# Optimization experiments

Measured on AMD Instinct MI355X. Metric: run time of the kernel, lower is better.

Reference implementation:

```python
import jax, jax.numpy as jnp
import numpy as np

VOCAB = 21128; EMBED = 768; D_MODEL = 256; H = 100; NTAGS = 21; B = 32; T = 256


def setup_inputs() -> dict:
    key = jax.random.key(0)
    ks = jax.random.split(key, 18)
    n = lambda k, s, sc=0.05: jax.random.normal(k, s, dtype=jnp.float32) * sc
    return {
        "words": jax.random.randint(ks[0], (B, T), 0, VOCAB),
        "target": jax.random.randint(ks[1], (B, T), 0, NTAGS),
        "embed_table": n(ks[2], (VOCAB, EMBED), 1.0),
        "in_fc_w": n(ks[3], (D_MODEL, EMBED)),
        "in_fc_b": n(ks[4], (D_MODEL,)),
        "Wih0": n(ks[5], (2, 4 * H, D_MODEL)),
        "Whh0": n(ks[6], (2, 4 * H, H)),
        "bih0": n(ks[7], (2, 4 * H)),
        "bhh0": n(ks[8], (2, 4 * H)),
        "Wih1": n(ks[9], (2, 4 * H, 2 * H)),
        "Whh1": n(ks[10], (2, 4 * H, H)),
        "bih1": n(ks[11], (2, 4 * H)),
        "bhh1": n(ks[12], (2, 4 * H)),
        "out_w": n(ks[13], (NTAGS, 2 * H)),
        "out_b": n(ks[14], (NTAGS,)),
        "trans": n(ks[15], (NTAGS, NTAGS)),
        "start_s": n(ks[16], (NTAGS,)),
        "end_s": n(ks[17], (NTAGS,)),
    }


def _lstm_dir(x, Wih, Whh, bih, bhh, reverse):
    # x: (T, B, D); torch LSTM gate order i, f, g, o
    Bsz, Hd = x.shape[1], Whh.shape[1]
    pre = jnp.einsum('tbd,gd->tbg', x, Wih) + bih  # precompute input projection

    def step(carry, p):
        h, c = carry
        g = p + h @ Whh.T + bhh
        i, f, gg, o = jnp.split(g, 4, axis=-1)
        c = jax.nn.sigmoid(f) * c + jax.nn.sigmoid(i) * jnp.tanh(gg)
        h = jax.nn.sigmoid(o) * jnp.tanh(c)
        return (h, c), h

    init = (jnp.zeros((Bsz, Hd), x.dtype), jnp.zeros((Bsz, Hd), x.dtype))
    _, hs = jax.lax.scan(step, init, pre, reverse=reverse)
    return hs


def _bilstm(x, layers):
    h = x
    for (Wih, Whh, bih, bhh) in layers:  # fixed small loop over num_layers
        f = _lstm_dir(h, Wih[0], Whh[0], bih[0], bhh[0], False)
        b = _lstm_dir(h, Wih[1], Whh[1], bih[1], bhh[1], True)
        h = jnp.concatenate([f, b], axis=-1)
    return h


def _crf_loss(logits, tags, mask, trans, start_s, end_s):
    # fastNLP ConditionalRandomField loss: normalizer - gold_score, per batch elem
    lt = jnp.swapaxes(logits, 0, 1)          # (T, B, N)
    tt = tags.T                               # (T, B)
    mt = mask.T.astype(logits.dtype)          # (T, B)
    alpha0 = lt[0] + start_s

    def step(alpha, inp):
        emit, m = inp
        tmp = alpha[:, :, None] + trans[None] + emit[:, None, :]  # (B, N, N)
        new = jax.nn.logsumexp(tmp, axis=1)
        return jnp.where(m[:, None] > 0, new, alpha), None

    alpha, _ = jax.lax.scan(step, alpha0, (lt[1:], mt[1:]))
    normalizer = jax.nn.logsumexp(alpha + end_s, axis=1)  # (B,)

    emit_sc = jnp.take_along_axis(lt, tt[..., None], axis=2)[..., 0] * mt
    trans_sc = trans[tt[:-1], tt[1:]] * mt[1:]
    seq_lens = mask.sum(axis=1)
    last_idx = jnp.maximum(seq_lens - 1, 0)
    last_tags = tags[jnp.arange(tags.shape[0]), last_idx]
    gold = emit_sc.sum(0) + trans_sc.sum(0) + start_s[tt[0]] + end_s[last_tags]
    return normalizer - gold


def reference(words, target, embed_table, in_fc_w, in_fc_b, Wih0, Whh0, bih0, bhh0,
              Wih1, Whh1, bih1, bhh1, out_w, out_b, trans, start_s, end_s):
    mask = words != 0
    x = embed_table[words]                       # (B, T, E)
    x = x @ in_fc_w.T + in_fc_b                  # (B, T, D)
    x = jnp.swapaxes(x, 0, 1)                    # (T, B, D)
    h = _bilstm(x, [(Wih0, Whh0, bih0, bhh0), (Wih1, Whh1, bih1, bhh1)])
    h = jnp.swapaxes(h, 0, 1)                    # (B, T, 2H); dropout is identity at eval
    logits = jax.nn.log_softmax(h @ out_w.T + out_b, axis=-1)
    return _crf_loss(logits, target, mask, trans, start_s, end_s)  # (B,)
```

## Files before the change

kernel.cpp:

```cpp
#include <hip/hip_runtime.h>
#include <hip/hip_bf16.h>

#define VOCAB 21128
#define EMBED 768
#define DMODEL 256
#define HID 100
#define NTAGS 21
#define BB 32
#define TT 256
#define NTOK (BB*TT)

typedef float f32x4 __attribute__((ext_vector_type(4)));
typedef unsigned int u32x4 __attribute__((ext_vector_type(4)));
typedef short s16x8 __attribute__((ext_vector_type(8)));

__device__ __forceinline__ float sigm(float x) { return 1.0f / (1.0f + __expf(-x)); }
__device__ __forceinline__ float tanh_(float x) { return 2.0f / (1.0f + __expf(-2.0f * x)) - 1.0f; }

__device__ __forceinline__ unsigned int bfr(float x) {
    unsigned int u = __float_as_uint(x);
    return (u + 0x7fffu + ((u >> 16) & 1u)) >> 16;
}
__device__ __forceinline__ unsigned int bfpack(float lo, float hi) {
    return (bfr(hi) << 16) | bfr(lo);
}
__device__ __forceinline__ s16x8 asfrag(u32x4 v) {
    union { u32x4 u; s16x8 s; } x; x.u = v; return x.s;
}

#define BAR() do { \
    asm volatile("s_waitcnt lgkmcnt(0)" ::: "memory"); \
    __builtin_amdgcn_s_barrier(); \
    __builtin_amdgcn_sched_barrier(0); \
} while (0)

__global__ __launch_bounds__(256) void gemm_mfma(
    const float* __restrict__ A, int lda,
    const float* __restrict__ B, int ldb,
    const float* __restrict__ bias1, const float* __restrict__ bias2,
    float* __restrict__ C, int ldc,
    int N, int K,
    const int* __restrict__ gatherWords, int permGates)
{
    __shared__ unsigned int As_[2][2048];
    __shared__ unsigned int Bs_[2][1024];

    const int tid = threadIdx.x;
    const int row0 = blockIdx.x * 128;
    const int col0 = blockIdx.y * 64;
    const int lane = tid & 63;
    const int wave = tid >> 6;
    const int wr = wave >> 1, wc = wave & 1;
    const int nsteps = (K + 31) >> 5;

    const float* arow[4]; int aoff[4]; int kqA[4];
    #pragma unroll
    for (int j = 0; j < 4; ++j) {
        int v = tid + 256 * j;
        int row = v >> 3, kq = v & 7;
        int grow = row0 + row;
        const float* ap;
        if (gatherWords) {
            int widx = gatherWords[(grow & 31) * TT + (grow >> 5)];
            ap = A + (size_t)widx * lda;
        } else {
            ap = A + (size_t)grow * lda;
        }
        arow[j] = ap + 4 * kq;
        aoff[j] = (row >> 4) * 256 + (kq >> 1) * 64 + (row & 15) * 4 + (kq & 1) * 2;
        kqA[j] = kq;
    }
    const float* brow[2]; int boff[2]; int bok[2]; int kqB[2];
    #pragma unroll
    for (int j = 0; j < 2; ++j) {
        int v = tid + 256 * j;
        int r = v >> 3, kq = v & 7;
        int gcol = col0 + r;
        bok[j] = (gcol < N);
        int src = bok[j] ? gcol : 0;
        if (permGates && bok[j]) {
            int d2 = (gcol >= 400) ? 1 : 0;
            int rr = gcol - d2 * 400;
            src = d2 * 400 + (rr & 3) * 100 + (rr >> 2);
        }
        brow[j] = B + (size_t)src * ldb + 4 * kq;
        boff[j] = (r >> 4) * 256 + (kq >> 1) * 64 + (r & 15) * 4 + (kq & 1) * 2;
        kqB[j] = kq;
    }

    {
        #pragma unroll
        for (int j = 0; j < 4; ++j) {
            f32x4 v = {0.f,0.f,0.f,0.f};
            if (4 * kqA[j] < K) v = *(const f32x4*)(arow[j]);
            As_[0][aoff[j]]     = bfpack(v.x, v.y);
            As_[0][aoff[j] + 1] = bfpack(v.z, v.w);
        }
        #pragma unroll
        for (int j = 0; j < 2; ++j) {
            f32x4 v = {0.f,0.f,0.f,0.f};
            if (bok[j] && 4 * kqB[j] < K) v = *(const f32x4*)(brow[j]);
            Bs_[0][boff[j]]     = bfpack(v.x, v.y);
            Bs_[0][boff[j] + 1] = bfpack(v.z, v.w);
        }
    }
    BAR();

    f32x4 acc[4][2] = {};

    for (int s = 0; s < nsteps; ++s) {
        const int cur = s & 1, nxt = cur ^ 1;

        f32x4 la[4], lb[2];
        if (s + 1 < nsteps) {
            const int kb = (s + 1) * 32;
            #pragma unroll
            for (int j = 0; j < 4; ++j) {
                la[j] = (f32x4){0.f,0.f,0.f,0.f};
                if (kb + 4 * kqA[j] < K) la[j] = *(const f32x4*)(arow[j] + kb);
            }
            #pragma unroll
            for (int j = 0; j < 2; ++j) {
                lb[j] = (f32x4){0.f,0.f,0.f,0.f};
                if (bok[j] && kb + 4 * kqB[j] < K) lb[j] = *(const f32x4*)(brow[j] + kb);
            }
        }

        u32x4 af[4], bf[2];
        #pragma unroll
        for (int mt = 0; mt < 4; ++mt)
            af[mt] = *(const u32x4*)&As_[cur][(4 * wr + mt) * 256 + lane * 4];
        #pragma unroll
        for (int nt = 0; nt < 2; ++nt)
            bf[nt] = *(const u32x4*)&Bs_[cur][(2 * wc + nt) * 256 + lane * 4];
        #pragma unroll
        for (int mt = 0; mt < 4; ++mt)
            #pragma unroll
            for (int nt = 0; nt < 2; ++nt)
                acc[mt][nt] = __builtin_amdgcn_mfma_f32_16x16x32_bf16(
                    asfrag(af[mt]), asfrag(bf[nt]), acc[mt][nt], 0, 0, 0);

        if (s + 1 < nsteps) {
            #pragma unroll
            for (int j = 0; j < 4; ++j) {
                As_[nxt][aoff[j]]     = bfpack(la[j].x, la[j].y);
                As_[nxt][aoff[j] + 1] = bfpack(la[j].z, la[j].w);
            }
            #pragma unroll
            for (int j = 0; j < 2; ++j) {
                Bs_[nxt][boff[j]]     = bfpack(lb[j].x, lb[j].y);
                Bs_[nxt][boff[j] + 1] = bfpack(lb[j].z, lb[j].w);
            }
        }
        BAR();
    }

    const int r4 = (lane >> 4) * 4;
    const int cl = lane & 15;
    #pragma unroll
    for (int nt = 0; nt < 2; ++nt) {
        int gcol = col0 + (2 * wc + nt) * 16 + cl;
        if (gcol < N) {
            int src = gcol;
            if (permGates) {
                int d2 = (gcol >= 400) ? 1 : 0;
                int rr = gcol - d2 * 400;
                src = d2 * 400 + (rr & 3) * 100 + (rr >> 2);
            }
            float bv = bias1[src];
            if (bias2) bv += bias2[src];
            #pragma unroll
            for (int mt = 0; mt < 4; ++mt) {
                int grow = row0 + (4 * wr + mt) * 16 + r4;
                #pragma unroll
                for (int r = 0; r < 4; ++r)
                    C[(size_t)(grow + r) * ldc + gcol] = acc[mt][nt][r] + bv;
            }
        }
    }
}

#define STASH_FRAG(DD, F, A0,A1,A2,A3) { \
    int tile = 4*wave + DD; if (tile > 24) tile = 24; \
    int row16 = 16*tile + m16; \
    const float* srcp = Whh + (size_t)(dir*400 + (row16 & 3)*100 + (row16 >> 2)) * HID; \
    const int k0 = 32*F + 8*g4; \
    f32x4 fa = {0.f,0.f,0.f,0.f}, fb = {0.f,0.f,0.f,0.f}; \
    if (k0 < HID) fa = *(const f32x4*)(srcp + k0); \
    if (k0 + 4 < HID) fb = *(const f32x4*)(srcp + k0 + 4); \
    unsigned p0 = bfpack(fa.x, fa.y), p1 = bfpack(fa.z, fa.w); \
    unsigned p2 = bfpack(fb.x, fb.y), p3 = bfpack(fb.z, fb.w); \
    asm volatile("v_accvgpr_write_b32 a" #A0 ", %0\n\t" \
                 "v_accvgpr_write_b32 a" #A1 ", %1\n\t" \
                 "v_accvgpr_write_b32 a" #A2 ", %2\n\t" \
                 "v_accvgpr_write_b32 a" #A3 ", %3" \
                 :: "v"(p0), "v"(p1), "v"(p2), "v"(p3) \
                 : "a" #A0, "a" #A1, "a" #A2, "a" #A3); }

#define MF(ACC, BF, A0, A3) \
    asm volatile("v_mfma_f32_16x16x32_bf16 %0, a[" #A0 ":" #A3 "], %1, %0" \
                 : "+v"(ACC) : "v"(BF));

#define LOADCHUNK(K2) { \
    const int s0_ = 16 * (K2); \
    _Pragma("unroll") \
    for (int j = 0; j < 4; ++j) { \
        if (okj[j]) { \
            int tg = dir ? (TT - 1 - (s0_ + sicj[j])) : (s0_ + sicj[j]); \
            rr[j] = *(const f32x4*)(pre + (size_t)(tg * BB + b) * 800 + dir * 400 + 4 * gqj[j]); \
        } \
    } }

#define WRITECHUNK(BUF) { \
    _Pragma("unroll") \
    for (int j = 0; j < 4; ++j) { \
        if (okj[j]) *(f32x4*)&preS[(BUF) * 6400 + sicj[j] * 400 + 4 * gqj[j]] = rr[j]; \
    } }

#define LSTM_STEP(SIC) { \
    const int t_ = dir ? (TT - 1 - (s0 + (SIC))) : (s0 + (SIC)); \
    const u32x4* hb_ = (const u32x4*)&h16[(SIC) & 1][0]; \
    u32x4 bf0 = hb_[g4], bf1 = hb_[4+g4], bf2 = hb_[8+g4], bf3 = hb_[12+g4]; \
    f32x4 p4 = *(const f32x4*)&preS[curbase + (SIC) * 400 + my_po]; \
    f32x4 acc0 = {0.f,0.f,0.f,0.f}, acc1 = {0.f,0.f,0.f,0.f}; \
    f32x4 acc2 = {0.f,0.f,0.f,0.f}, acc3 = {0.f,0.f,0.f,0.f}; \
    asm volatile("s_nop 1"); \
    MF(acc0, bf0, 0, 3)   MF(acc1, bf0, 16, 19) MF(acc2, bf0, 32, 35) MF(acc3, bf0, 48, 51) \
    MF(acc0, bf1, 4, 7)   MF(acc1, bf1, 20, 23) MF(acc2, bf1, 36, 39) MF(acc3, bf1, 52, 55) \
    MF(acc0, bf2, 8, 11)  MF(acc1, bf2, 24, 27) MF(acc2, bf2, 40, 43) MF(acc3, bf2, 56, 59) \
    MF(acc0, bf3, 12, 15) MF(acc1, bf3, 28, 31) MF(acc2, bf3, 44, 47) MF(acc3, bf3, 60, 63) \
    asm volatile("s_nop 7\n\ts_nop 7"); \
    f32x4 sel = (d == 0) ? acc0 : (d == 1) ? acc1 : (d == 2) ? acc2 : acc3; \
    float igt = sigm(sel.x + p4.x); \
    float fgt = sigm(sel.y + p4.y); \
    float ggt = tanh_(sel.z + p4.z); \
    float ogt = sigm(sel.w + p4.w); \
    c = fgt * c + igt * ggt; \
    float h = ogt * tanh_(c); \
    if (writer) { \
        h16[((SIC) + 1) & 1][my_u] = (unsigned short)bfr(h); \
        hout[(size_t)(t_ * BB + b) * 200 + dir * HID + my_u] = h; \
    } \
    BAR(); }

__global__ __launch_bounds__(448, 1) void lstm_mfma(
    const float* __restrict__ pre,
    const float* __restrict__ Whh,
    float* __restrict__ hout)
{
    const int dir = blockIdx.x >> 5;
    const int b = blockIdx.x & 31;
    const int tid = threadIdx.x;
    const int wave = tid >> 6;
    const int lane = tid & 63;
    const int m16 = lane & 15;
    const int g4 = lane >> 4;
    const int d = lane & 3;

    __shared__ alignas(16) unsigned short h16[2][128];
    __shared__ alignas(16) float preS[2 * 6400];

    STASH_FRAG(0,0, 0,1,2,3)    STASH_FRAG(0,1, 4,5,6,7)
    STASH_FRAG(0,2, 8,9,10,11)  STASH_FRAG(0,3, 12,13,14,15)
    STASH_FRAG(1,0, 16,17,18,19) STASH_FRAG(1,1, 20,21,22,23)
    STASH_FRAG(1,2, 24,25,26,27) STASH_FRAG(1,3, 28,29,30,31)
    STASH_FRAG(2,0, 32,33,34,35) STASH_FRAG(2,1, 36,37,38,39)
    STASH_FRAG(2,2, 40,41,42,43) STASH_FRAG(2,3, 44,45,46,47)
    STASH_FRAG(3,0, 48,49,50,51) STASH_FRAG(3,1, 52,53,54,55)
    STASH_FRAG(3,2, 56,57,58,59) STASH_FRAG(3,3, 60,61,62,63)

    if (tid < 128) { h16[0][tid] = 0; h16[1][tid] = 0; }

    int my_tile = 4 * wave + d; if (my_tile > 24) my_tile = 24;
    const int my_u = my_tile * 4 + g4;
    const int my_po = 16 * my_tile + 4 * g4;
    const bool writer = ((lane & 12) == 0) && (wave < 6 || d == 0);

    int sicj[4], gqj[4]; bool okj[4];
    #pragma unroll
    for (int j = 0; j < 4; ++j) {
        int idx = tid + 448 * j;
        okj[j] = (idx < 1600);
        int ic = okj[j] ? idx : 0;
        sicj[j] = ic / 100;
        gqj[j] = ic - 100 * sicj[j];
    }

    float c = 0.f;
    f32x4 rr[4];

    LOADCHUNK(0)
    WRITECHUNK(0)
    LOADCHUNK(1)
    BAR();

    for (int k = 0; k < 16; ++k) {
        const int s0 = 16 * k;
        const int curbase = (k & 1) * 6400;
        LSTM_STEP(0)  LSTM_STEP(1)  LSTM_STEP(2)  LSTM_STEP(3)
        LSTM_STEP(4)  LSTM_STEP(5)  LSTM_STEP(6)  LSTM_STEP(7)
        LSTM_STEP(8)  LSTM_STEP(9)  LSTM_STEP(10) LSTM_STEP(11)
        LSTM_STEP(12) LSTM_STEP(13) LSTM_STEP(14) LSTM_STEP(15)
        if (k < 15) { WRITECHUNK((k & 1) ^ 1) }
        if (k < 14) { LOADCHUNK(k + 2) }
        BAR();
    }
}

__global__ __launch_bounds__(256) void logits_lsm(
    const float* __restrict__ h1,
    const float* __restrict__ out_w,
    const float* __restrict__ out_b,
    float* __restrict__ logits)
{
    const int lane = threadIdx.x & 63;
    const int wid = (blockIdx.x * 256 + threadIdx.x) >> 6;
    const int half = lane >> 5;
    const int n = lane & 31;
    const int i = wid * 2 + half;
    if (i >= NTOK) return;

    float acc = -1e30f;
    if (n < NTAGS) {
        acc = out_b[n];
        const float4* hr = (const float4*)(h1 + (size_t)i * 200);
        const float4* wr = (const float4*)(out_w + (size_t)n * 200);
        #pragma unroll
        for (int e = 0; e < 50; ++e) {
            float4 h4 = hr[e], w4 = wr[e];
            acc += h4.x * w4.x + h4.y * w4.y + h4.z * w4.z + h4.w * w4.w;
        }
    }
    float m = acc;
    for (int off = 16; off > 0; off >>= 1) m = fmaxf(m, __shfl_xor(m, off, 32));
    float ex = (n < NTAGS) ? __expf(acc - m) : 0.f;
    float s = ex;
    for (int off = 16; off > 0; off >>= 1) s += __shfl_xor(s, off, 32);
    if (n < NTAGS) logits[(size_t)i * NTAGS + n] = acc - m - __logf(s);
}

__global__ __launch_bounds__(64) void crf_kernel(
    const float* __restrict__ logits,
    const int* __restrict__ words,
    const int* __restrict__ target,
    const float* __restrict__ trans,
    const float* __restrict__ start_s,
    const float* __restrict__ end_s,
    float* __restrict__ out)
{
    const int b = blockIdx.x;
    const int j = threadIdx.x;

    float tcol[NTAGS];
    #pragma unroll
    for (int i = 0; i < NTAGS; ++i) tcol[i] = (j < NTAGS) ? trans[i * NTAGS + j] : 0.f;

    float alpha = (j < NTAGS) ? (logits[(size_t)(0 * BB + b) * NTAGS + j] + start_s[j]) : -1e30f;

    for (int t = 1; t < TT; ++t) {
        bool mt = (words[b * TT + t] != 0);
        if (mt) {
            float v[NTAGS];
            float mx = -1e30f;
            #pragma unroll
            for (int i2 = 0; i2 < NTAGS; ++i2) {
                float ai = __shfl(alpha, i2, 64);
                v[i2] = ai + tcol[i2];
                mx = fmaxf(mx, v[i2]);
            }
            float s = 0.f;
            #pragma unroll
            for (int i2 = 0; i2 < NTAGS; ++i2) s += __expf(v[i2] - mx);
            float na = mx + __logf(s) + logits[(size_t)(t * BB + b) * NTAGS + j];
            alpha = (j < NTAGS) ? na : -1e30f;
        }
    }

    float val = (j < NTAGS) ? (alpha + end_s[j]) : -1e30f;
    float mx = val;
    for (int off = 32; off > 0; off >>= 1) mx = fmaxf(mx, __shfl_xor(mx, off, 64));
    float s = (j < NTAGS) ? __expf(val - mx) : 0.f;
    for (int off = 32; off > 0; off >>= 1) s += __shfl_xor(s, off, 64);
    float norm = mx + __logf(s);

    float gold = 0.f, slen = 0.f;
    for (int t = j; t < TT; t += 64) {
        int tg = target[b * TT + t];
        bool m = (words[b * TT + t] != 0);
        if (m) {
            gold += logits[(size_t)(t * BB + b) * NTAGS + tg];
            slen += 1.f;
            if (t >= 1) gold += trans[target[b * TT + t - 1] * NTAGS + tg];
        }
    }
    for (int off = 32; off > 0; off >>= 1) {
        gold += __shfl_xor(gold, off, 64);
        slen += __shfl_xor(slen, off, 64);
    }
    if (j == 0) {
        int len = (int)slen;
        int last = (len > 0) ? (len - 1) : 0;
        int last_tag = target[b * TT + last];
        gold += start_s[target[b * TT + 0]] + end_s[last_tag];
        out[b] = norm - gold;
    }
}

extern "C" void kernel_launch(void* const* d_in, const int* in_sizes, int n_in,
                              void* d_out, int out_size, void* d_ws, size_t ws_size,
                              hipStream_t stream) {
    const int*   words   = (const int*)  d_in[0];
    const int*   target  = (const int*)  d_in[1];
    const float* embed   = (const float*)d_in[2];
    const float* in_fc_w = (const float*)d_in[3];
    const float* in_fc_b = (const float*)d_in[4];
    const float* Wih0    = (const float*)d_in[5];
    const float* Whh0    = (const float*)d_in[6];
    const float* bih0    = (const float*)d_in[7];
    const float* bhh0    = (const float*)d_in[8];
    const float* Wih1    = (const float*)d_in[9];
    const float* Whh1    = (const float*)d_in[10];
    const float* bih1    = (const float*)d_in[11];
    const float* bhh1    = (const float*)d_in[12];
    const float* out_w   = (const float*)d_in[13];
    const float* out_b   = (const float*)d_in[14];
    const float* trans   = (const float*)d_in[15];
    const float* start_s = (const float*)d_in[16];
    const float* end_s   = (const float*)d_in[17];
    float* out = (float*)d_out;

    float* ws = (float*)d_ws;
    float* x      = ws;
    float* pre    = ws + 2097152;
    float* h0     = ws + 8650752;
    float* h1     = ws;
    float* logits = ws + 1638400;

    gemm_mfma<<<dim3(64, 4), 256, 0, stream>>>(
        embed, EMBED, in_fc_w, EMBED, in_fc_b, nullptr,
        x, DMODEL, DMODEL, EMBED, words, 0);

    gemm_mfma<<<dim3(64, 13), 256, 0, stream>>>(
        x, DMODEL, Wih0, DMODEL, bih0, bhh0,
        pre, 800, 800, DMODEL, nullptr, 1);

    lstm_mfma<<<64, 448, 0, stream>>>(pre, Whh0, h0);

    gemm_mfma<<<dim3(64, 13), 256, 0, stream>>>(
        h0, 200, Wih1, 200, bih1, bhh1,
        pre, 800, 800, 200, nullptr, 1);

    lstm_mfma<<<64, 448, 0, stream>>>(pre, Whh1, h1);

    logits_lsm<<<NTOK / 8, 256, 0, stream>>>(h1, out_w, out_b, logits);

    crf_kernel<<<BB, 64, 0, stream>>>(logits, words, target, trans, start_s, end_s, out);
}
```

Baseline: 580.6 us.

## Deepen GEMM K-tile, restructure CRF recurrence, template LSTM barrier variant

The GEMM now stages 64-wide K slices instead of 32, halving the number of barrier-separated steps and doubling the MFMAs issued per step, at the cost of double the LDS and more registers. The CRF forward recursion preloads the word mask into registers, prefetches the next timestep's emission, and replaces serial max/sum chains with tree reductions to shorten the dependent latency per step. The LSTM kernel is templated so the second-layer launch drops the sched_barrier after each step's barrier, letting the compiler schedule across it.

```diff
diff --git a/kernel.cpp b/kernel.cpp
--- a/kernel.cpp
+++ b/kernel.cpp
@@ -28,11 +28,12 @@
     union { u32x4 u; s16x8 s; } x; x.u = v; return x.s;
 }
 
-#define BAR() do { \
+#define BARV(SB) do { \
     asm volatile("s_waitcnt lgkmcnt(0)" ::: "memory"); \
     __builtin_amdgcn_s_barrier(); \
-    __builtin_amdgcn_sched_barrier(0); \
+    if (SB) __builtin_amdgcn_sched_barrier(0); \
 } while (0)
+#define BAR() BARV(1)
 
 __global__ __launch_bounds__(256) void gemm_mfma(
     const float* __restrict__ A, int lda,
@@ -42,8 +43,8 @@
     int N, int K,
     const int* __restrict__ gatherWords, int permGates)
 {
-    __shared__ unsigned int As_[2][2048];
-    __shared__ unsigned int Bs_[2][1024];
+    __shared__ unsigned int As_[2][4096];
+    __shared__ unsigned int Bs_[2][2048];
 
     const int tid = threadIdx.x;
     const int row0 = blockIdx.x * 128;
@@ -51,13 +52,13 @@
     const int lane = tid & 63;
     const int wave = tid >> 6;
     const int wr = wave >> 1, wc = wave & 1;
-    const int nsteps = (K + 31) >> 5;
-
-    const float* arow[4]; int aoff[4]; int kqA[4];
+    const int nsteps = (K + 63) >> 6;
+
+    const float* arow[8]; int aoff[8]; int kqA[8];
     #pragma unroll
-    for (int j = 0; j < 4; ++j) {
+    for (int j = 0; j < 8; ++j) {
         int v = tid + 256 * j;
-        int row = v >> 3, kq = v & 7;
+        int row = v >> 4, kq = v & 15;
         int grow = row0 + row;
         const float* ap;
         if (gatherWords) {
@@ -67,14 +68,15 @@
             ap = A + (size_t)grow * lda;
         }
         arow[j] = ap + 4 * kq;
-        aoff[j] = (row >> 4) * 256 + (kq >> 1) * 64 + (row & 15) * 4 + (kq & 1) * 2;
+        aoff[j] = (row >> 4) * 512 + (kq >> 3) * 256 + ((kq >> 1) & 3) * 64
+                + (row & 15) * 4 + (kq & 1) * 2;
         kqA[j] = kq;
     }
-    const float* brow[2]; int boff[2]; int bok[2]; int kqB[2];
+    const float* brow[4]; int boff[4]; int bok[4]; int kqB[4];
     #pragma unroll
-    for (int j = 0; j < 2; ++j) {
+    for (int j = 0; j < 4; ++j) {
         int v = tid + 256 * j;
-        int r = v >> 3, kq = v & 7;
+        int r = v >> 4, kq = v & 15;
         int gcol = col0 + r;
         bok[j] = (gcol < N);
         int src = bok[j] ? gcol : 0;
@@ -84,20 +86,21 @@
             src = d2 * 400 + (rr & 3) * 100 + (rr >> 2);
         }
         brow[j] = B + (size_t)src * ldb + 4 * kq;
-        boff[j] = (r >> 4) * 256 + (kq >> 1) * 64 + (r & 15) * 4 + (kq & 1) * 2;
+        boff[j] = (r >> 4) * 512 + (kq >> 3) * 256 + ((kq >> 1) & 3) * 64
+                + (r & 15) * 4 + (kq & 1) * 2;
         kqB[j] = kq;
     }
 
     {
         #pragma unroll
-        for (int j = 0; j < 4; ++j) {
+        for (int j = 0; j < 8; ++j) {
             f32x4 v = {0.f,0.f,0.f,0.f};
             if (4 * kqA[j] < K) v = *(const f32x4*)(arow[j]);
             As_[0][aoff[j]]     = bfpack(v.x, v.y);
             As_[0][aoff[j] + 1] = bfpack(v.z, v.w);
         }
         #pragma unroll
-        for (int j = 0; j < 2; ++j) {
+        for (int j = 0; j < 4; ++j) {
             f32x4 v = {0.f,0.f,0.f,0.f};
             if (bok[j] && 4 * kqB[j] < K) v = *(const f32x4*)(brow[j]);
             Bs_[0][boff[j]]     = bfpack(v.x, v.y);
@@ -111,43 +114,48 @@
     for (int s = 0; s < nsteps; ++s) {
         const int cur = s & 1, nxt = cur ^ 1;
 
-        f32x4 la[4], lb[2];
+        f32x4 la[8], lb[4];
         if (s + 1 < nsteps) {
-            const int kb = (s + 1) * 32;
-            #pragma unroll
-            for (int j = 0; j < 4; ++j) {
+            const int kb = (s + 1) * 64;
+            #pragma unroll
+            for (int j = 0; j < 8; ++j) {
                 la[j] = (f32x4){0.f,0.f,0.f,0.f};
                 if (kb + 4 * kqA[j] < K) la[j] = *(const f32x4*)(arow[j] + kb);
             }
             #pragma unroll
-            for (int j = 0; j < 2; ++j) {
+            for (int j = 0; j < 4; ++j) {
                 lb[j] = (f32x4){0.f,0.f,0.f,0.f};
                 if (bok[j] && kb + 4 * kqB[j] < K) lb[j] = *(const f32x4*)(brow[j] + kb);
             }
         }
 
-        u32x4 af[4], bf[2];
+        u32x4 af[2][4], bf2[2][2];
         #pragma unroll
-        for (int mt = 0; mt < 4; ++mt)
-            af[mt] = *(const u32x4*)&As_[cur][(4 * wr + mt) * 256 + lane * 4];
+        for (int f = 0; f < 2; ++f) {
+            #pragma unroll
+            for (int mt = 0; mt < 4; ++mt)
+                af[f][mt] = *(const u32x4*)&As_[cur][(4 * wr + mt) * 512 + f * 256 + lane * 4];
+            #pragma unroll
+            for (int nt = 0; nt < 2; ++nt)
+                bf2[f][nt] = *(const u32x4*)&Bs_[cur][(2 * wc + nt) * 512 + f * 256 + lane * 4];
+        }
         #pragma unroll
-        for (int nt = 0; nt < 2; ++nt)
-            bf[nt] = *(const u32x4*)&Bs_[cur][(2 * wc + nt) * 256 + lane * 4];
-        #pragma unroll
-        for (int mt = 0; mt < 4; ++mt)
-            #pragma unroll
-            for (int nt = 0; nt < 2; ++nt)
-                acc[mt][nt] = __builtin_amdgcn_mfma_f32_16x16x32_bf16(
-                    asfrag(af[mt]), asfrag(bf[nt]), acc[mt][nt], 0, 0, 0);
+        for (int f = 0; f < 2; ++f)
+            #pragma unroll
+            for (int mt = 0; mt < 4; ++mt)
+                #pragma unroll
+                for (int nt = 0; nt < 2; ++nt)
+                    acc[mt][nt] = __builtin_amdgcn_mfma_f32_16x16x32_bf16(
+                        asfrag(af[f][mt]), asfrag(bf2[f][nt]), acc[mt][nt], 0, 0, 0);
 
         if (s + 1 < nsteps) {
             #pragma unroll
-            for (int j = 0; j < 4; ++j) {
+            for (int j = 0; j < 8; ++j) {
                 As_[nxt][aoff[j]]     = bfpack(la[j].x, la[j].y);
                 As_[nxt][aoff[j] + 1] = bfpack(la[j].z, la[j].w);
             }
             #pragma unroll
-            for (int j = 0; j < 2; ++j) {
+            for (int j = 0; j < 4; ++j) {
                 Bs_[nxt][boff[j]]     = bfpack(lb[j].x, lb[j].y);
                 Bs_[nxt][boff[j] + 1] = bfpack(lb[j].z, lb[j].w);
             }
@@ -219,6 +227,7 @@
 
 #define LSTM_STEP(SIC) { \
     const int t_ = dir ? (TT - 1 - (s0 + (SIC))) : (s0 + (SIC)); \
+    const int i_ = t_ * BB + b; \
     const u32x4* hb_ = (const u32x4*)&h16[(SIC) & 1][0]; \
     u32x4 bf0 = hb_[g4], bf1 = hb_[4+g4], bf2 = hb_[8+g4], bf3 = hb_[12+g4]; \
     f32x4 p4 = *(const f32x4*)&preS[curbase + (SIC) * 400 + my_po]; \
@@ -239,10 +248,11 @@
     float h = ogt * tanh_(c); \
     if (writer) { \
         h16[((SIC) + 1) & 1][my_u] = (unsigned short)bfr(h); \
-        hout[(size_t)(t_ * BB + b) * 200 + dir * HID + my_u] = h; \
+        hout[(size_t)i_ * 200 + dir * HID + my_u] = h; \
     } \
-    BAR(); }
-
+    BARV(VAR == 0); }
+
+template<int VAR>
 __global__ __launch_bounds__(448, 1) void lstm_mfma(
     const float* __restrict__ pre,
     const float* __restrict__ Whh,
@@ -350,31 +360,63 @@
 {
     const int b = blockIdx.x;
     const int j = threadIdx.x;
+    const int j21 = (j < NTAGS) ? j : (NTAGS - 1);
 
     float tcol[NTAGS];
     #pragma unroll
     for (int i = 0; i < NTAGS; ++i) tcol[i] = (j < NTAGS) ? trans[i * NTAGS + j] : 0.f;
 
+    const int w0 = words[b * TT +   0 + j];
+    const int w1 = words[b * TT +  64 + j];
+    const int w2 = words[b * TT + 128 + j];
+    const int w3 = words[b * TT + 192 + j];
+
     float alpha = (j < NTAGS) ? (logits[(size_t)(0 * BB + b) * NTAGS + j] + start_s[j]) : -1e30f;
-
-    for (int t = 1; t < TT; ++t) {
-        bool mt = (words[b * TT + t] != 0);
-        if (mt) {
-            float v[NTAGS];
-            float mx = -1e30f;
-            #pragma unroll
-            for (int i2 = 0; i2 < NTAGS; ++i2) {
-                float ai = __shfl(alpha, i2, 64);
-                v[i2] = ai + tcol[i2];
-                mx = fmaxf(mx, v[i2]);
-            }
-            float s = 0.f;
-            #pragma unroll
-            for (int i2 = 0; i2 < NTAGS; ++i2) s += __expf(v[i2] - mx);
-            float na = mx + __logf(s) + logits[(size_t)(t * BB + b) * NTAGS + j];
-            alpha = (j < NTAGS) ? na : -1e30f;
-        }
-    }
+    float e_cur = logits[(size_t)(1 * BB + b) * NTAGS + j21];
+
+#define CRF_CHUNK(WREG, T0) \
+    for (int u = ((T0) == 0 ? 1 : 0); u < 64; ++u) { \
+        const int t = (T0) + u; \
+        float e_nxt = 0.f; \
+        if (t + 1 < TT) e_nxt = logits[(size_t)((t + 1) * BB + b) * NTAGS + j21]; \
+        if (__shfl(WREG, u, 64) != 0) { \
+            float v[NTAGS]; \
+            _Pragma("unroll") \
+            for (int i2 = 0; i2 < NTAGS; ++i2) \
+                v[i2] = __shfl(alpha, i2, 64) + tcol[i2]; \
+            float m0[11]; \
+            _Pragma("unroll") \
+            for (int p = 0; p < 10; ++p) m0[p] = fmaxf(v[2*p], v[2*p+1]); \
+            m0[10] = v[20]; \
+            float m1[6]; \
+            _Pragma("unroll") \
+            for (int p = 0; p < 5; ++p) m1[p] = fmaxf(m0[2*p], m0[2*p+1]); \
+            m1[5] = m0[10]; \
+            float m2a = fmaxf(m1[0], m1[1]), m2b = fmaxf(m1[2], m1[3]), m2c = fmaxf(m1[4], m1[5]); \
+            float mx = fmaxf(fmaxf(m2a, m2b), m2c); \
+            float e[NTAGS]; \
+            _Pragma("unroll") \
+            for (int i2 = 0; i2 < NTAGS; ++i2) e[i2] = __expf(v[i2] - mx); \
+            float s0[11]; \
+            _Pragma("unroll") \
+            for (int p = 0; p < 10; ++p) s0[p] = e[2*p] + e[2*p+1]; \
+            s0[10] = e[20]; \
+            float s1[6]; \
+            _Pragma("unroll") \
+            for (int p = 0; p < 5; ++p) s1[p] = s0[2*p] + s0[2*p+1]; \
+            s1[5] = s0[10]; \
+            float ss = ((s1[0] + s1[1]) + (s1[2] + s1[3])) + (s1[4] + s1[5]); \
+            float na = mx + __logf(ss) + e_cur; \
+            alpha = (j < NTAGS) ? na : -1e30f; \
+        } \
+        e_cur = e_nxt; \
+    }
+
+    CRF_CHUNK(w0, 0)
+    CRF_CHUNK(w1, 64)
+    CRF_CHUNK(w2, 128)
+    CRF_CHUNK(w3, 192)
+#undef CRF_CHUNK
 
     float val = (j < NTAGS) ? (alpha + end_s[j]) : -1e30f;
     float mx = val;
@@ -444,13 +486,13 @@
         x, DMODEL, Wih0, DMODEL, bih0, bhh0,
         pre, 800, 800, DMODEL, nullptr, 1);
 
-    lstm_mfma<<<64, 448, 0, stream>>>(pre, Whh0, h0);
+    lstm_mfma<0><<<64, 448, 0, stream>>>(pre, Whh0, h0);
 
     gemm_mfma<<<dim3(64, 13), 256, 0, stream>>>(
         h0, 200, Wih1, 200, bih1, bhh1,
         pre, 800, 800, 200, nullptr, 1);
 
-    lstm_mfma<<<64, 448, 0, stream>>>(pre, Whh1, h1);
+    lstm_mfma<1><<<64, 448, 0, stream>>>(pre, Whh1, h1);
 
     logits_lsm<<<NTOK / 8, 256, 0, stream>>>(h1, out_w, out_b, logits);
 
```

After: 582.6 us. No clear change (+0.3%).
